# Performance work log

Hardware: AMD Instinct MI355X
Metric: run time of the kernel (lower is better)

The kernel has to match this reference:

```python
import jax, jax.numpy as jnp
import numpy as np

B, T, C, H, HS = 2, 2048, 1024, 16, 64
W_SIZE = 128
BLK = 64
NB = T // BLK            # 32 blocks
NSEL = 8                 # selected blocks per (b, h)
EPS = 1e-8


def setup_inputs() -> dict:
    key = jax.random.key(0)
    ks = jax.random.split(key, 12)
    s = 0.02
    return {
        "hidden_states": jax.random.normal(ks[0], (B, T, C), dtype=jnp.float32),
        "Wq": jax.random.normal(ks[1], (C, C), dtype=jnp.float32) * s,
        "bq": jnp.zeros((C,), jnp.float32),
        "Wk": jax.random.normal(ks[2], (C, C), dtype=jnp.float32) * s,
        "bk": jnp.zeros((C,), jnp.float32),
        "Wv": jax.random.normal(ks[3], (C, C), dtype=jnp.float32) * s,
        "bv": jnp.zeros((C,), jnp.float32),
        "Wo": jax.random.normal(ks[4], (C, C), dtype=jnp.float32) * s,
        "bo": jnp.zeros((C,), jnp.float32),
        "Wg": jax.random.normal(ks[5], (C, 3), dtype=jnp.float32) * s,
        "bg": jnp.zeros((3,), jnp.float32),
    }


def _sdpa(q, k, v, mask):
    # q: [B,H,Tq,HS], k/v: [B,H,S,HS], mask: [Tq,S] bool (True = attend)
    scale = 1.0 / jnp.sqrt(jnp.asarray(HS, q.dtype))
    scores = jnp.einsum('bhqd,bhkd->bhqk', q, k) * scale
    scores = jnp.where(mask, scores, jnp.asarray(-jnp.inf, scores.dtype))
    return jnp.einsum('bhqk,bhkd->bhqd', jax.nn.softmax(scores, axis=-1), v)


def _forward(x, Wq, bq, Wk, bk, Wv, bv, Wo, bo, Wg, bg):
    q = (x @ Wq + bq).reshape(B, T, H, HS).transpose(0, 2, 1, 3)
    k = (x @ Wk + bk).reshape(B, T, H, HS).transpose(0, 2, 1, 3)
    v = (x @ Wv + bv).reshape(B, T, H, HS).transpose(0, 2, 1, 3)

    gates = jax.nn.softmax(x @ Wg + bg, axis=-1)  # [B,T,3]
    g_sl, g_sel, g_cmp = gates[..., 0:1], gates[..., 1:2], gates[..., 2:3]

    i = jnp.arange(T)[:, None]

    # --- sliding-window branch (causal AND within window band) ---
    j = jnp.arange(T)[None, :]
    slide_mask = (j <= i) & (i - j <= W_SIZE)
    out_sl = _sdpa(q, k, v, slide_mask)

    # --- block representatives (mean-pooled K/V blocks) ---
    kb = k.reshape(B, H, NB, BLK, HS)
    vb = v.reshape(B, H, NB, BLK, HS)
    k_rep = kb.mean(axis=3)  # [B,H,NB,HS]

    # cosine similarity of each query vs each block rep, averaged over T
    qn = q / jnp.maximum(jnp.linalg.norm(q, axis=-1, keepdims=True), EPS)
    kn = k_rep / jnp.maximum(jnp.linalg.norm(k_rep, axis=-1, keepdims=True), EPS)
    global_scores = jnp.einsum('bhtd,bhnd->bhtn', qn, kn).mean(axis=2)  # [B,H,NB]
    _, top_idx = jax.lax.top_k(global_scores, NSEL)  # [B,H,NSEL]

    # gather selected K/V blocks
    sel_k = jnp.take_along_axis(kb, top_idx[..., None, None], axis=2).reshape(B, H, NSEL * BLK, HS)
    sel_v = jnp.take_along_axis(vb, top_idx[..., None, None], axis=2).reshape(B, H, NSEL * BLK, HS)

    # torch is_causal with Tq != S is top-left aligned: allow j <= i
    js = jnp.arange(NSEL * BLK)[None, :]
    out_sel = _sdpa(q, sel_k, sel_v, js <= i)

    # --- compressed branch over block reps ---
    v_cmp = vb.mean(axis=3)  # [B,H,NB,HS]
    jc = jnp.arange(NB)[None, :]
    out_cmp = _sdpa(q, k_rep, v_cmp, jc <= i)

    def merge(o):
        return o.transpose(0, 2, 1, 3).reshape(B, T, C)

    out = g_sl * merge(out_sl) + g_sel * merge(out_sel) + g_cmp * merge(out_cmp)
    return out @ Wo + bo


def reference(hidden_states, Wq, bq, Wk, bk, Wv, bv, Wo, bo, Wg, bg):
    return _forward(hidden_states, Wq, bq, Wk, bk, Wv, bv, Wo, bo, Wg, bg)
```

## Files before the change

kernel.cpp:

```cpp
#include <hip/hip_runtime.h>
#include <hip/hip_bf16.h>
#include <math.h>

#define Bc   2
#define Tc   2048
#define Cc   1024
#define Hc   16
#define HSc  64
#define WSZ  128
#define BLKc 64
#define NBc  32
#define NSELc 8
#define Mrows (Bc*Tc)
#define QCH  32
#define LST  88
#define LSTP 68
#define MAXT 12
#define SOFT_C 4.0f

typedef __attribute__((ext_vector_type(8))) _Float16 half8;
typedef __attribute__((ext_vector_type(4))) float f32x4v;
typedef __attribute__((ext_vector_type(8))) unsigned short ushort8v;

__device__ __forceinline__ float wave_sum(float v) {
    #pragma unroll
    for (int o = 32; o; o >>= 1) v += __shfl_xor(v, o);
    return v;
}

__device__ __forceinline__ unsigned short f2h(float f) {
    _Float16 h = (_Float16)f;
    unsigned short u;
    __builtin_memcpy(&u, &h, 2);
    return u;
}
__device__ __forceinline__ float h2f(unsigned short u) {
    _Float16 h;
    __builtin_memcpy(&h, &u, 2);
    return (float)h;
}

__device__ __forceinline__ void gload16(const void* g, void* l) {
    __builtin_amdgcn_global_load_lds(
        (const __attribute__((address_space(1))) void*)g,
        (__attribute__((address_space(3))) void*)l, 16, 0, 0);
}

__global__ __launch_bounds__(256)
void cvt_gates_kernel(const float* __restrict__ x, unsigned short* __restrict__ xb,
                      const float* __restrict__ Wg, const float* __restrict__ bg,
                      float* __restrict__ gates)
{
    if (blockIdx.x < 4096) {
        int i = (blockIdx.x * 256 + threadIdx.x) * 4;
        float4 v = *(const float4*)&x[i];
        ushort4 o;
        o.x = f2h(v.x); o.y = f2h(v.y); o.z = f2h(v.z); o.w = f2h(v.w);
        *(ushort4*)&xb[i] = o;
        return;
    }
    const int row  = (blockIdx.x - 4096) * 4 + (threadIdx.x >> 6);
    const int lane = threadIdx.x & 63;
    const float* xr = x + (size_t)row * Cc;
    float p0 = 0, p1 = 0, p2 = 0;
    #pragma unroll
    for (int it = 0; it < 4; ++it) {
        int k4 = lane * 4 + it * 256;
        float4 xv = *(const float4*)&xr[k4];
        float4 w0 = *(const float4*)&Wg[k4 * 3];
        float4 w1 = *(const float4*)&Wg[k4 * 3 + 4];
        float4 w2 = *(const float4*)&Wg[k4 * 3 + 8];
        p0 += xv.x * w0.x + xv.y * w0.w + xv.z * w1.z + xv.w * w2.y;
        p1 += xv.x * w0.y + xv.y * w1.x + xv.z * w1.w + xv.w * w2.z;
        p2 += xv.x * w0.z + xv.y * w1.y + xv.z * w2.x + xv.w * w2.w;
    }
    p0 = wave_sum(p0); p1 = wave_sum(p1); p2 = wave_sum(p2);
    if (lane == 0) {
        p0 += bg[0]; p1 += bg[1]; p2 += bg[2];
        float m = fmaxf(p0, fmaxf(p1, p2));
        float e0 = expf(p0 - m), e1 = expf(p1 - m), e2 = expf(p2 - m);
        float s = e0 + e1 + e2;
        gates[row * 3 + 0] = e0 / s;
        gates[row * 3 + 1] = e1 / s;
        gates[row * 3 + 2] = e2 / s;
    }
}

__global__ __launch_bounds__(256)
void cvt_wT4_kernel(const float* __restrict__ W0, const float* __restrict__ W1,
                    const float* __restrict__ W2, const float* __restrict__ W3,
                    unsigned short* __restrict__ D012, unsigned short* __restrict__ D3)
{
    __shared__ float tile[64][65];
    const int z = blockIdx.z;
    const float* W = (z == 0) ? W0 : (z == 1) ? W1 : (z == 2) ? W2 : W3;
    unsigned short* WT = (z < 3) ? (D012 + (size_t)z * 1024 * 1024) : D3;
    const int n0 = blockIdx.x * 64, k0 = blockIdx.y * 64;
    const int tid = threadIdx.x;
    #pragma unroll
    for (int it = 0; it < 16; ++it) {
        int lin = tid + it * 256;
        int r = lin >> 6, c = lin & 63;
        tile[r][c] = W[(size_t)(k0 + r) * 1024 + n0 + c];
    }
    __syncthreads();
    #pragma unroll
    for (int it = 0; it < 16; ++it) {
        int lin = tid + it * 256;
        int n = lin >> 6, k = lin & 63;
        WT[(size_t)(n0 + n) * 1024 + k0 + k] = f2h(tile[k][n]);
    }
}


#define FENCE asm volatile("" ::: "memory")
#define BAR() do { FENCE; __builtin_amdgcn_s_barrier(); FENCE; } while(0)
#define WAIT_LGKM0() do { asm volatile("s_waitcnt lgkmcnt(0)" ::: "memory"); \
                          __builtin_amdgcn_sched_barrier(0); } while(0)
#define WAIT_VM(N) do { asm volatile("s_waitcnt vmcnt(" #N ")" ::: "memory"); } while(0)

#define LDA(BUF, MH) do { \
    const unsigned short* _p = &lds[BUF][0][(wmo + (MH)*64 + r16) * 64]; \
    a0[0] = *(const half8*)(_p +        cc0); a1[0] = *(const half8*)(_p +        cc1); \
    a0[1] = *(const half8*)(_p + 1024 + cc0); a1[1] = *(const half8*)(_p + 1024 + cc1); \
    a0[2] = *(const half8*)(_p + 2048 + cc0); a1[2] = *(const half8*)(_p + 2048 + cc1); \
    a0[3] = *(const half8*)(_p + 3072 + cc0); a1[3] = *(const half8*)(_p + 3072 + cc1); \
} while(0)

#define LDB(BUF, NH) do { \
    const unsigned short* _p = &lds[BUF][1][(wno + (NH)*32 + r16) * 64]; \
    b0[0] = *(const half8*)(_p +        cc0); b1[0] = *(const half8*)(_p +        cc1); \
    b0[1] = *(const half8*)(_p + 1024 + cc0); b1[1] = *(const half8*)(_p + 1024 + cc1); \
} while(0)

#define CLP(I, J, MH, NH) \
    acc[(MH)*4+(I)][(NH)*2+(J)] = __builtin_amdgcn_mfma_f32_16x16x32_f16(a0[I], b0[J], acc[(MH)*4+(I)][(NH)*2+(J)], 0, 0, 0); \
    acc[(MH)*4+(I)][(NH)*2+(J)] = __builtin_amdgcn_mfma_f32_16x16x32_f16(a1[I], b1[J], acc[(MH)*4+(I)][(NH)*2+(J)], 0, 0, 0);
#define CL(MH, NH) do { \
    __builtin_amdgcn_s_setprio(1); \
    CLP(0,0,MH,NH) CLP(0,1,MH,NH) CLP(1,0,MH,NH) CLP(1,1,MH,NH) \
    CLP(2,0,MH,NH) CLP(2,1,MH,NH) CLP(3,0,MH,NH) CLP(3,1,MH,NH) \
    __builtin_amdgcn_s_setprio(0); \
} while(0)

#define STAGEA(BUF, G, TILE) do { \
    size_t _co = (size_t)(TILE) * 64 + scol_x; \
    gload16(Ag + (size_t)(m0 +       (G)*64 + wid*8 + l8) * 1024 + _co, \
            &lds[BUF][0][((G)*64 + wid*8) * 64]); \
    gload16(Ag + (size_t)(m0 + 128 + (G)*64 + wid*8 + l8) * 1024 + _co, \
            &lds[BUF][0][(128 + (G)*64 + wid*8) * 64]); \
} while(0)

#define STAGEB(BUF, G, TILE) do { \
    size_t _co = (size_t)(TILE) * 64 + scol_x; \
    int _r0 = (wid >> 2) * 64 + (G)*32 + (wid & 3) * 8; \
    gload16(BTg + (size_t)(n0 +       _r0 + l8) * 1024 + _co, \
            &lds[BUF][1][_r0 * 64]); \
    gload16(BTg + (size_t)(n0 + 128 + _r0 + l8) * 1024 + _co, \
            &lds[BUF][1][(128 + _r0) * 64]); \
} while(0)

__global__ __launch_bounds__(512, 2)
void mfma_gemm_qkv8(const unsigned short* __restrict__ Ag,
                    const unsigned short* __restrict__ BTg,
                    const float* __restrict__ bq, const float* __restrict__ bk,
                    const float* __restrict__ bv,
                    unsigned short* __restrict__ Qh, unsigned short* __restrict__ Kf,
                    unsigned short* __restrict__ Vf)
{
    __shared__ unsigned short lds[2][2][256 * 64];
    const int tid  = threadIdx.x;
    const int lane = tid & 63, wid = tid >> 6;
    const int quad = lane >> 4, r16 = lane & 15;
    const int m0 = blockIdx.y * 256, n0 = blockIdx.x * 256;
    const int wmo = (wid >> 2) * 128;
    const int wno = (wid & 3) * 64;
    const int l8 = lane >> 3;
    const int scol_x = ((lane & 7) ^ l8) * 8;
    const int xsw = (r16 & 7) * 8;
    const int cc0 = (quad * 8) ^ xsw;
    const int cc1 = (32 + quad * 8) ^ xsw;

    f32x4v acc[8][4];
    #pragma unroll
    for (int i = 0; i < 8; ++i)
        #pragma unroll
        for (int j = 0; j < 4; ++j)
            acc[i][j] = (f32x4v){0.f, 0.f, 0.f, 0.f};

    half8 a0[4], a1[4], b0[2], b1[2];

    STAGEA(0, 0, 0); STAGEB(0, 1, 0); STAGEA(0, 1, 0); STAGEB(0, 0, 0);
    STAGEA(1, 0, 1); STAGEB(1, 1, 1);
    WAIT_VM(4);
    BAR();

    for (int it = 0; it < 8; ++it) {
        const int t1 = 2 * it + 1, t2v = 2 * it + 2, t3v = 2 * it + 3;
        const bool s2 = (t2v < 16), s3 = (t3v < 16);
        LDA(0, 0); LDB(0, 0);
        STAGEA(1, 1, t1);
        BAR(); WAIT_LGKM0();
        CL(0, 0);
        BAR();
        LDB(0, 1);
        STAGEB(1, 0, t1);
        BAR(); WAIT_LGKM0();
        CL(0, 1);
        BAR();
        LDA(0, 1);
        if (s2) STAGEA(0, 0, t2v);
        BAR(); WAIT_LGKM0();
        CL(1, 1);
        BAR();
        LDB(0, 0);
        if (s2) STAGEB(0, 1, t2v);
        BAR(); WAIT_LGKM0();
        CL(1, 0);
        if (it == 7) { WAIT_VM(0); } else { WAIT_VM(4); }
        BAR();
        LDA(1, 0); LDB(1, 0);
        if (s2) STAGEA(0, 1, t2v);
        BAR(); WAIT_LGKM0();
        CL(0, 0);
        BAR();
        LDB(1, 1);
        if (s2) STAGEB(0, 0, t2v);
        BAR(); WAIT_LGKM0();
        CL(0, 1);
        BAR();
        LDA(1, 1);
        if (s3) STAGEA(1, 0, t3v);
        BAR(); WAIT_LGKM0();
        CL(1, 1);
        BAR();
        LDB(1, 0);
        if (s3) STAGEB(1, 1, t3v);
        BAR(); WAIT_LGKM0();
        CL(1, 0);
        if (it < 7) WAIT_VM(4);
        BAR();
    }

    const int which = n0 >> 10;
    const float* bias = (which == 0) ? bq : ((which == 1) ? bk : bv);
    unsigned short* dst = (which == 0) ? Qh : ((which == 1) ? Kf : Vf);
    const float sc = (which == 0) ? 0.125f : 1.0f;
    #pragma unroll
    for (int i = 0; i < 8; ++i) {
        int mbase = m0 + wmo + i * 16 + quad * 4;
        #pragma unroll
        for (int j = 0; j < 4; ++j) {
            int n = n0 + wno + j * 16 + r16;
            int nn = n & 1023;
            float bvv = bias[nn];
            int h = nn >> 6, d = nn & 63;
            #pragma unroll
            for (int r = 0; r < 4; ++r) {
                int m = mbase + r;
                int b = m >> 11, t = m & 2047;
                float v = (acc[i][j][r] + bvv) * sc;
                dst[(((size_t)(b * Hc + h) * Tc) + t) * HSc + d] = f2h(v);
            }
        }
    }
}

__global__ __launch_bounds__(256)
void mfma_gemm_kernel(const unsigned short* __restrict__ A,
                      const unsigned short* __restrict__ BT,
                      const float* __restrict__ bias,
                      float* __restrict__ Y)
{
    constexpr int K = 1024;
    __shared__ unsigned short As[4 * 64 * 8];
    __shared__ unsigned short Bs[4 * 128 * 8];
    const int tid  = threadIdx.x;
    const int lane = tid & 63;
    const int wid  = tid >> 6;
    const int m0 = blockIdx.y * 64, n0 = blockIdx.x * 128;
    const int wm = (wid >> 1) * 32, wn = (wid & 1) * 64;

    f32x4v acc[2][4];
    #pragma unroll
    for (int i = 0; i < 2; ++i)
        #pragma unroll
        for (int j = 0; j < 4; ++j)
            acc[i][j] = (f32x4v){0.f, 0.f, 0.f, 0.f};

    const int kq_r = lane >> 4;
    const int r16  = lane & 15;

    for (int k0 = 0; k0 < K; k0 += 32) {
        __syncthreads();
        gload16(A + (size_t)(m0 + lane) * K + k0 + wid * 8,
                As + (size_t)(wid * 64) * 8);
        #pragma unroll
        for (int it = 0; it < 2; ++it) {
            int cell = wid * 64 + it * 256 + lane;
            int kq = cell >> 7, row = cell & 127;
            gload16(BT + (size_t)(n0 + row) * K + k0 + kq * 8,
                    Bs + (size_t)(wid * 64 + it * 256) * 8);
        }
        __syncthreads();

        half8 af[2], bf[4];
        #pragma unroll
        for (int i = 0; i < 2; ++i)
            af[i] = *(const half8*)&As[(size_t)(kq_r * 64 + wm + i * 16 + r16) * 8];
        #pragma unroll
        for (int j = 0; j < 4; ++j)
            bf[j] = *(const half8*)&Bs[(size_t)(kq_r * 128 + wn + j * 16 + r16) * 8];
        #pragma unroll
        for (int i = 0; i < 2; ++i)
            #pragma unroll
            for (int j = 0; j < 4; ++j)
                acc[i][j] = __builtin_amdgcn_mfma_f32_16x16x32_f16(af[i], bf[j], acc[i][j], 0, 0, 0);
    }

    #pragma unroll
    for (int i = 0; i < 2; ++i) {
        int mbase = m0 + wm + i * 16 + (lane >> 4) * 4;
        #pragma unroll
        for (int j = 0; j < 4; ++j) {
            int n = n0 + wn + j * 16 + (lane & 15);
            float bv = bias[n];
            #pragma unroll
            for (int r = 0; r < 4; ++r)
                Y[(size_t)(mbase + r) * 1024 + n] = acc[i][j][r] + bv;
        }
    }
}

__global__ __launch_bounds__(256)
void vtrans_stats_kernel(const unsigned short* __restrict__ Kf,
                         const unsigned short* __restrict__ Vf,
                         unsigned short* __restrict__ Vt,
                         float* __restrict__ krep,
                         unsigned short* __restrict__ krep16,
                         unsigned short* __restrict__ vcmpT16)
{
    __shared__ unsigned short vtile[64][65];
    __shared__ unsigned short ktile[64][65];
    const int nb = blockIdx.x, bh = blockIdx.y;
    const int t0 = nb * BLKc;
    const int tid = threadIdx.x;
    const int c4 = (tid & 15) * 4, r = tid >> 4;
    const unsigned short* vsrc = Vf + ((size_t)bh * Tc + t0) * HSc;
    const unsigned short* ksrc = Kf + ((size_t)bh * Tc + t0) * HSc;
    #pragma unroll
    for (int it = 0; it < 4; ++it) {
        int tt = r + it * 16;
        *(ushort4*)&vtile[tt][c4] = *(const ushort4*)&vsrc[(size_t)tt * HSc + c4];
        *(ushort4*)&ktile[tt][c4] = *(const ushort4*)&ksrc[(size_t)tt * HSc + c4];
    }
    __syncthreads();
    unsigned short* dst = Vt + (size_t)bh * HSc * Tc + t0;
    #pragma unroll
    for (int it = 0; it < 4; ++it) {
        int d = r + it * 16;
        ushort4 o;
        o.x = vtile[c4 + 0][d]; o.y = vtile[c4 + 1][d];
        o.z = vtile[c4 + 2][d]; o.w = vtile[c4 + 3][d];
        *(ushort4*)&dst[(size_t)d * Tc + c4] = o;
    }
    if (tid < 64) {
        const int d = tid;
        float sk = 0.f, sv = 0.f;
        #pragma unroll 8
        for (int t = 0; t < BLKc; ++t) {
            sk += h2f(ktile[t][d]);
            sv += h2f(vtile[t][d]);
        }
        float km = sk * (1.0f / BLKc), vm = sv * (1.0f / BLKc);
        krep[((size_t)bh * NBc + nb) * HSc + d] = km;
        krep16[(size_t)bh * 4096 + nb * 64 + d] = f2h(km);
        krep16[(size_t)bh * 4096 + (nb + 32) * 64 + d] = 0;
        vcmpT16[(size_t)bh * 4096 + d * 64 + nb] = f2h(vm);
        vcmpT16[(size_t)bh * 4096 + d * 64 + nb + 32] = 0;
    }
}

__global__ __launch_bounds__(64)
void qbar_part_kernel(const unsigned short* __restrict__ Qh, float* __restrict__ qpart)
{
    __shared__ float rinv[64];
    const int ch = blockIdx.x, bh = blockIdx.y, lane = threadIdx.x;
    const int t0 = ch * (Tc / QCH);
    const unsigned short* qbase = Qh + ((size_t)bh * Tc + t0) * HSc;

    {
        const unsigned short* qr = qbase + (size_t)lane * HSc;
        float ss = 0.f;
        #pragma unroll
        for (int d8 = 0; d8 < 8; ++d8) {
            ushort8v v8 = *(const ushort8v*)&qr[d8 * 8];
            #pragma unroll
            for (int j = 0; j < 8; ++j) { float f = h2f(v8[j]); ss += f * f; }
        }
        rinv[lane] = 1.0f / fmaxf(sqrtf(ss), 1e-8f);
    }
    __syncthreads();

    float acc = 0.f;
    #pragma unroll 8
    for (int t = 0; t < 64; ++t)
        acc += h2f(qbase[(size_t)t * HSc + lane]) * rinv[t];
    qpart[((size_t)bh * QCH + ch) * HSc + lane] = acc;
}

__global__ __launch_bounds__(64)
void topk_kernel(const float* __restrict__ qpart, const float* __restrict__ krep,
                 int* __restrict__ topidx)
{
    int bh = blockIdx.x, lane = threadIdx.x;
    __shared__ float sc[NBc];
    __shared__ float qbs[HSc];
    float qa = 0.0f;
    #pragma unroll
    for (int c = 0; c < QCH; c++)
        qa += qpart[((size_t)bh * QCH + c) * HSc + lane];
    qbs[lane] = qa * (1.0f / Tc);
    __syncthreads();
    if (lane < NBc) {
        float dot = 0, nk = 0;
        for (int d = 0; d < HSc; d++) {
            float kv = krep[((size_t)bh * NBc + lane) * HSc + d];
            nk += kv * kv;
            dot += qbs[d] * kv;
        }
        sc[lane] = dot / fmaxf(sqrtf(nk), 1e-8f);
    }
    __syncthreads();
    if (lane == 0) {
        for (int s = 0; s < NSELc; s++) {
            int best = 0; float bv = sc[0];
            for (int n = 1; n < NBc; n++)
                if (sc[n] > bv) { bv = sc[n]; best = n; }
            topidx[bh * NSELc + s] = best;
            sc[best] = -INFINITY;
        }
    }
}

__device__ __forceinline__ void attn_tile3(
    int p0, int wlim, int klim, int qg0,
    const unsigned short* __restrict__ Kh, const unsigned short* __restrict__ Vt,
    unsigned short* __restrict__ Ph,
    half8 aq0, half8 aq1, half8 ones, int wq, int l16, int quad,
    f32x4v o[4], f32x4v& o5)
{
    f32x4v s[4];
    #pragma unroll
    for (int t = 0; t < 4; ++t) {
        f32x4v sa = (f32x4v){0.f, 0.f, 0.f, 0.f};
        half8 b0 = *(const half8*)&Kh[(t * 16 + l16) * LST + quad * 8];
        half8 b1 = *(const half8*)&Kh[(t * 16 + l16) * LST + 32 + quad * 8];
        sa = __builtin_amdgcn_mfma_f32_16x16x32_f16(aq0, b0, sa, 0, 0, 0);
        sa = __builtin_amdgcn_mfma_f32_16x16x32_f16(aq1, b1, sa, 0, 0, 0);
        s[t] = sa;
    }

    #pragma unroll
    for (int t = 0; t < 4; ++t) {
        int kk = t * 16 + l16;
        bool kok = kk < klim;
        int jt = p0 + kk;
        #pragma unroll
        for (int r = 0; r < 4; ++r) {
            int q = qg0 + r;
            bool valid = kok && (jt <= q) && (q - jt <= wlim);
            float p = valid ? __expf(s[t][r] - SOFT_C) : 0.0f;
            Ph[(wq + quad * 4 + r) * LSTP + t * 16 + l16] = f2h(p);
        }
    }


    half8 ap0 = *(const half8*)&Ph[(wq + l16) * LSTP + quad * 8];
    half8 ap1 = *(const half8*)&Ph[(wq + l16) * LSTP + 32 + quad * 8];
    o5 = __builtin_amdgcn_mfma_f32_16x16x32_f16(ap0, ones, o5, 0, 0, 0);
    o5 = __builtin_amdgcn_mfma_f32_16x16x32_f16(ap1, ones, o5, 0, 0, 0);
    #pragma unroll
    for (int dt = 0; dt < 4; ++dt) {
        half8 v0 = *(const half8*)&Vt[(dt * 16 + l16) * LST + quad * 8];
        half8 v1 = *(const half8*)&Vt[(dt * 16 + l16) * LST + 32 + quad * 8];
        o[dt] = __builtin_amdgcn_mfma_f32_16x16x32_f16(ap0, v0, o[dt], 0, 0, 0);
        o[dt] = __builtin_amdgcn_mfma_f32_16x16x32_f16(ap1, v1, o[dt], 0, 0, 0);
    }
}

__global__ __launch_bounds__(256)
void fattn_kernel(const unsigned short* __restrict__ Qh16,
                  const unsigned short* __restrict__ Kf,
                  const unsigned short* __restrict__ Vtg,
                  const unsigned short* __restrict__ krep16,
                  const unsigned short* __restrict__ vcmpT16,
                  const int* __restrict__ topidx,
                  const float* __restrict__ gates, unsigned short* __restrict__ merged)
{
    __shared__ unsigned short KH[2][64 * LST];
    __shared__ unsigned short VT[2][64 * LST];
    __shared__ unsigned short Ph[64 * LSTP];
    __shared__ float gsl[3 * 64];
    __shared__ int tKb[MAXT], tP0[MAXT], tWl[MAXT], tKl[MAXT], tBid[MAXT];

    const int qt = blockIdx.x;
    const int bh = blockIdx.y;
    const int b  = bh >> 4, h = bh & 15;
    const int tid  = threadIdx.x;
    const int wid  = tid >> 6, lane = tid & 63;
    const int l16  = lane & 15, quad = lane >> 4;
    const int q0 = qt * 64;
    const int wq = wid * 16;
    const int qg0 = q0 + wq + quad * 4;

    const int nslide = (qt < 2 ? qt : 2) + 1;
    const int nsel   = (qt + 1 < NSELc) ? (qt + 1) : NSELc;
    const int nt     = nslide + nsel + 1;

    half8 aq0, aq1, ones;
    {
        const unsigned short* qrow = Qh16 + ((size_t)bh * Tc + q0 + wq + l16) * HSc;
        aq0 = *(const half8*)(qrow + quad * 8);
        aq1 = *(const half8*)(qrow + 32 + quad * 8);
        #pragma unroll
        for (int j = 0; j < 8; ++j) ones[j] = (_Float16)1.0f;
    }

    if (tid < 64) {
        size_t gb = ((size_t)b * Tc + q0 + tid) * 3;
        gsl[0 * 64 + tid] = gates[gb + 0];
        gsl[1 * 64 + tid] = gates[gb + 1];
        gsl[2 * 64 + tid] = gates[gb + 2];
    }
    if (tid < nt) {
        int i = tid, kb, p0, wl, kl, bid;
        if (i < nslide)            { int tb = q0 - (nslide - 1 - i) * 64;
                                     kb = tb; p0 = tb; wl = WSZ; kl = 64; bid = 0; }
        else if (i < nslide + nsel){ int s = i - nslide;
                                     kb = topidx[bh * NSELc + s] * BLKc;
                                     p0 = s * BLKc; wl = 1 << 30; kl = 64; bid = 1; }
        else                       { kb = 0; p0 = 0; wl = 1 << 30; kl = NBc; bid = 2; }
        tKb[i] = kb; tP0[i] = p0; tWl[i] = wl; tKl[i] = kl; tBid[i] = bid;
    }

    f32x4v o[4], macc[4];
    f32x4v o5 = (f32x4v){0.f, 0.f, 0.f, 0.f};
    #pragma unroll
    for (int dt = 0; dt < 4; ++dt) {
        o[dt]    = (f32x4v){0.f, 0.f, 0.f, 0.f};
        macc[dt] = (f32x4v){0.f, 0.f, 0.f, 0.f};
    }

    const int seg = tid & 7, r0 = tid >> 3;
    const unsigned short* kbh = Kf  + (size_t)bh * Tc * HSc;
    const unsigned short* vbh = Vtg + (size_t)bh * HSc * Tc;

    {
        int tb0 = q0 - (nslide - 1) * 64;
        const unsigned short* kp = kbh + (size_t)tb0 * HSc;
        const unsigned short* vp = vbh + tb0;
        ushort8v k0 = *(const ushort8v*)(kp + (size_t)r0 * HSc + seg * 8);
        ushort8v k1 = *(const ushort8v*)(kp + (size_t)(r0 + 32) * HSc + seg * 8);
        ushort8v v0 = *(const ushort8v*)(vp + (size_t)r0 * Tc + seg * 8);
        ushort8v v1 = *(const ushort8v*)(vp + (size_t)(r0 + 32) * Tc + seg * 8);
        *(ushort8v*)&KH[0][r0 * LST + seg * 8] = k0;
        *(ushort8v*)&KH[0][(r0 + 32) * LST + seg * 8] = k1;
        *(ushort8v*)&VT[0][r0 * LST + seg * 8] = v0;
        *(ushort8v*)&VT[0][(r0 + 32) * LST + seg * 8] = v1;
    }
    __syncthreads();

    int pb = 0;
    for (int i = 0; i < nt; ++i) {
        const int cb = i & 1;
        const bool pf = (i + 1 < nt);
        ushort8v k0, k1, v0, v1;
        if (pf) {
            int bid2 = tBid[i + 1], kb2 = tKb[i + 1];
            const unsigned short *kp, *vp;
            int vs;
            if (bid2 < 2) { kp = kbh + (size_t)kb2 * HSc; vp = vbh + kb2; vs = Tc; }
            else          { kp = krep16 + (size_t)bh * 4096;
                            vp = vcmpT16 + (size_t)bh * 4096; vs = 64; }
            k0 = *(const ushort8v*)(kp + (size_t)r0 * HSc + seg * 8);
            k1 = *(const ushort8v*)(kp + (size_t)(r0 + 32) * HSc + seg * 8);
            v0 = *(const ushort8v*)(vp + (size_t)r0 * vs + seg * 8);
            v1 = *(const ushort8v*)(vp + (size_t)(r0 + 32) * vs + seg * 8);
        }
        int bid = tBid[i];
        if (bid != pb) {
            #pragma unroll
            for (int r = 0; r < 4; ++r) {
                float inv = gsl[pb * 64 + wq + quad * 4 + r] / o5[r];
                #pragma unroll
                for (int dt = 0; dt < 4; ++dt) { macc[dt][r] += inv * o[dt][r]; o[dt][r] = 0.f; }
                o5[r] = 0.f;
            }
            pb = bid;
        }
        attn_tile3(tP0[i], tWl[i], tKl[i], qg0, KH[cb], VT[cb], Ph,
                   aq0, aq1, ones, wq, l16, quad, o, o5);
        if (pf) {
            *(ushort8v*)&KH[cb ^ 1][r0 * LST + seg * 8] = k0;
            *(ushort8v*)&KH[cb ^ 1][(r0 + 32) * LST + seg * 8] = k1;
            *(ushort8v*)&VT[cb ^ 1][r0 * LST + seg * 8] = v0;
            *(ushort8v*)&VT[cb ^ 1][(r0 + 32) * LST + seg * 8] = v1;
        }
        __syncthreads();
    }
    #pragma unroll
    for (int r = 0; r < 4; ++r) {
        float inv = gsl[pb * 64 + wq + quad * 4 + r] / o5[r];
        #pragma unroll
        for (int dt = 0; dt < 4; ++dt) macc[dt][r] += inv * o[dt][r];
    }

    #pragma unroll
    for (int r = 0; r < 4; ++r) {
        size_t mrow = (size_t)b * Tc + qg0 + r;
        #pragma unroll
        for (int dt = 0; dt < 4; ++dt)
            merged[mrow * Cc + h * HSc + dt * 16 + l16] = f2h(macc[dt][r]);
    }
}

extern "C" void kernel_launch(void* const* d_in, const int* in_sizes, int n_in,
                              void* d_out, int out_size, void* d_ws, size_t ws_size,
                              hipStream_t stream)
{
    const float* x  = (const float*)d_in[0];
    const float* Wq = (const float*)d_in[1];
    const float* bq = (const float*)d_in[2];
    const float* Wk = (const float*)d_in[3];
    const float* bk = (const float*)d_in[4];
    const float* Wv = (const float*)d_in[5];
    const float* bv = (const float*)d_in[6];
    const float* Wo = (const float*)d_in[7];
    const float* bo = (const float*)d_in[8];
    const float* Wg = (const float*)d_in[9];
    const float* bg = (const float*)d_in[10];
    float* out = (float*)d_out;
    float* ws  = (float*)d_ws;

    unsigned short* Qh16 = (unsigned short*)(ws + 0);
    unsigned short* Kf16 = (unsigned short*)(ws + 2097152);
    unsigned short* Vf16 = (unsigned short*)(ws + 4194304);
    unsigned short* Vt16 = (unsigned short*)(ws + 6291456);
    unsigned short* Mgb  = (unsigned short*)(ws + 8388608);
    unsigned short* xb   = (unsigned short*)(ws + 10485760);
    unsigned short* WqkvT = (unsigned short*)(ws + 12582912);
    unsigned short* WoT   = (unsigned short*)(ws + 14155776);
    float* gates = ws + 14680064;
    float* krep  = ws + 14692352;
    unsigned short* krep16  = (unsigned short*)(ws + 14757888);
    unsigned short* vcmpT16 = (unsigned short*)(ws + 14823424);
    float* qpart = ws + 14888960;
    int*   topidx = (int*)(ws + 14954496);

    cvt_gates_kernel<<<4096 + Mrows / 4, 256, 0, stream>>>(x, xb, Wg, bg, gates);
    cvt_wT4_kernel<<<dim3(16, 16, 4), 256, 0, stream>>>(Wq, Wk, Wv, Wo, WqkvT, WoT);

    mfma_gemm_qkv8<<<dim3(12, 16), 512, 0, stream>>>(xb, WqkvT, bq, bk, bv,
                                                     Qh16, Kf16, Vf16);
    vtrans_stats_kernel<<<dim3(NBc, Bc * Hc), 256, 0, stream>>>(Kf16, Vf16, Vt16,
                                                                krep, krep16, vcmpT16);
    qbar_part_kernel<<<dim3(QCH, Bc * Hc), 64, 0, stream>>>(Qh16, qpart);
    topk_kernel<<<Bc * Hc, 64, 0, stream>>>(qpart, krep, topidx);
    fattn_kernel<<<dim3(Tc / 64, Bc * Hc), 256, 0, stream>>>(Qh16, Kf16, Vt16,
                                                             krep16, vcmpT16,
                                                             topidx, gates, Mgb);
    mfma_gemm_kernel<<<dim3(8, 64), 256, 0, stream>>>(Mgb, WoT, bo, out);
}
```

Measured before the change: 233.9 us.

## Load attention K/V fragments directly from global memory into registers

Removes the shared-memory double-buffered K/V staging and the per-tile block-wide barriers from the fused attention kernel. Each wave now loads its MFMA operand fragments for K and V straight from global memory (relying on L1/L2 for reuse across the four waves), computes the tile descriptors inline, and reads gates directly. Occupancy is raised via launch bounds and smaller LDS. The trade is redundant global loads per wave and no explicit prefetch overlap, with load latency exposed before each tile's MFMAs.

```diff
diff --git a/kernel.cpp b/kernel.cpp
--- a/kernel.cpp
+++ b/kernel.cpp
@@ -13,9 +13,7 @@
 #define NSELc 8
 #define Mrows (Bc*Tc)
 #define QCH  32
-#define LST  88
 #define LSTP 68
-#define MAXT 12
 #define SOFT_C 4.0f
 
 typedef __attribute__((ext_vector_type(8))) _Float16 half8;
@@ -443,53 +441,7 @@
     }
 }
 
-__device__ __forceinline__ void attn_tile3(
-    int p0, int wlim, int klim, int qg0,
-    const unsigned short* __restrict__ Kh, const unsigned short* __restrict__ Vt,
-    unsigned short* __restrict__ Ph,
-    half8 aq0, half8 aq1, half8 ones, int wq, int l16, int quad,
-    f32x4v o[4], f32x4v& o5)
-{
-    f32x4v s[4];
-    #pragma unroll
-    for (int t = 0; t < 4; ++t) {
-        f32x4v sa = (f32x4v){0.f, 0.f, 0.f, 0.f};
-        half8 b0 = *(const half8*)&Kh[(t * 16 + l16) * LST + quad * 8];
-        half8 b1 = *(const half8*)&Kh[(t * 16 + l16) * LST + 32 + quad * 8];
-        sa = __builtin_amdgcn_mfma_f32_16x16x32_f16(aq0, b0, sa, 0, 0, 0);
-        sa = __builtin_amdgcn_mfma_f32_16x16x32_f16(aq1, b1, sa, 0, 0, 0);
-        s[t] = sa;
-    }
-
-    #pragma unroll
-    for (int t = 0; t < 4; ++t) {
-        int kk = t * 16 + l16;
-        bool kok = kk < klim;
-        int jt = p0 + kk;
-        #pragma unroll
-        for (int r = 0; r < 4; ++r) {
-            int q = qg0 + r;
-            bool valid = kok && (jt <= q) && (q - jt <= wlim);
-            float p = valid ? __expf(s[t][r] - SOFT_C) : 0.0f;
-            Ph[(wq + quad * 4 + r) * LSTP + t * 16 + l16] = f2h(p);
-        }
-    }
-
-
-    half8 ap0 = *(const half8*)&Ph[(wq + l16) * LSTP + quad * 8];
-    half8 ap1 = *(const half8*)&Ph[(wq + l16) * LSTP + 32 + quad * 8];
-    o5 = __builtin_amdgcn_mfma_f32_16x16x32_f16(ap0, ones, o5, 0, 0, 0);
-    o5 = __builtin_amdgcn_mfma_f32_16x16x32_f16(ap1, ones, o5, 0, 0, 0);
-    #pragma unroll
-    for (int dt = 0; dt < 4; ++dt) {
-        half8 v0 = *(const half8*)&Vt[(dt * 16 + l16) * LST + quad * 8];
-        half8 v1 = *(const half8*)&Vt[(dt * 16 + l16) * LST + 32 + quad * 8];
-        o[dt] = __builtin_amdgcn_mfma_f32_16x16x32_f16(ap0, v0, o[dt], 0, 0, 0);
-        o[dt] = __builtin_amdgcn_mfma_f32_16x16x32_f16(ap1, v1, o[dt], 0, 0, 0);
-    }
-}
-
-__global__ __launch_bounds__(256)
+__global__ __launch_bounds__(256, 3)
 void fattn_kernel(const unsigned short* __restrict__ Qh16,
                   const unsigned short* __restrict__ Kf,
                   const unsigned short* __restrict__ Vtg,
@@ -498,11 +450,7 @@
                   const int* __restrict__ topidx,
                   const float* __restrict__ gates, unsigned short* __restrict__ merged)
 {
-    __shared__ unsigned short KH[2][64 * LST];
-    __shared__ unsigned short VT[2][64 * LST];
     __shared__ unsigned short Ph[64 * LSTP];
-    __shared__ float gsl[3 * 64];
-    __shared__ int tKb[MAXT], tP0[MAXT], tWl[MAXT], tKl[MAXT], tBid[MAXT];
 
     const int qt = blockIdx.x;
     const int bh = blockIdx.y;
@@ -527,23 +475,6 @@
         for (int j = 0; j < 8; ++j) ones[j] = (_Float16)1.0f;
     }
 
-    if (tid < 64) {
-        size_t gb = ((size_t)b * Tc + q0 + tid) * 3;
-        gsl[0 * 64 + tid] = gates[gb + 0];
-        gsl[1 * 64 + tid] = gates[gb + 1];
-        gsl[2 * 64 + tid] = gates[gb + 2];
-    }
-    if (tid < nt) {
-        int i = tid, kb, p0, wl, kl, bid;
-        if (i < nslide)            { int tb = q0 - (nslide - 1 - i) * 64;
-                                     kb = tb; p0 = tb; wl = WSZ; kl = 64; bid = 0; }
-        else if (i < nslide + nsel){ int s = i - nslide;
-                                     kb = topidx[bh * NSELc + s] * BLKc;
-                                     p0 = s * BLKc; wl = 1 << 30; kl = 64; bid = 1; }
-        else                       { kb = 0; p0 = 0; wl = 1 << 30; kl = NBc; bid = 2; }
-        tKb[i] = kb; tP0[i] = p0; tWl[i] = wl; tKl[i] = kl; tBid[i] = bid;
-    }
-
     f32x4v o[4], macc[4];
     f32x4v o5 = (f32x4v){0.f, 0.f, 0.f, 0.f};
     #pragma unroll
@@ -552,66 +483,89 @@
         macc[dt] = (f32x4v){0.f, 0.f, 0.f, 0.f};
     }
 
-    const int seg = tid & 7, r0 = tid >> 3;
     const unsigned short* kbh = Kf  + (size_t)bh * Tc * HSc;
     const unsigned short* vbh = Vtg + (size_t)bh * HSc * Tc;
-
-    {
-        int tb0 = q0 - (nslide - 1) * 64;
-        const unsigned short* kp = kbh + (size_t)tb0 * HSc;
-        const unsigned short* vp = vbh + tb0;
-        ushort8v k0 = *(const ushort8v*)(kp + (size_t)r0 * HSc + seg * 8);
-        ushort8v k1 = *(const ushort8v*)(kp + (size_t)(r0 + 32) * HSc + seg * 8);
-        ushort8v v0 = *(const ushort8v*)(vp + (size_t)r0 * Tc + seg * 8);
-        ushort8v v1 = *(const ushort8v*)(vp + (size_t)(r0 + 32) * Tc + seg * 8);
-        *(ushort8v*)&KH[0][r0 * LST + seg * 8] = k0;
-        *(ushort8v*)&KH[0][(r0 + 32) * LST + seg * 8] = k1;
-        *(ushort8v*)&VT[0][r0 * LST + seg * 8] = v0;
-        *(ushort8v*)&VT[0][(r0 + 32) * LST + seg * 8] = v1;
-    }
-    __syncthreads();
+    const int lofs = l16 * 64 + quad * 8;
 
     int pb = 0;
     for (int i = 0; i < nt; ++i) {
-        const int cb = i & 1;
-        const bool pf = (i + 1 < nt);
-        ushort8v k0, k1, v0, v1;
-        if (pf) {
-            int bid2 = tBid[i + 1], kb2 = tKb[i + 1];
-            const unsigned short *kp, *vp;
-            int vs;
-            if (bid2 < 2) { kp = kbh + (size_t)kb2 * HSc; vp = vbh + kb2; vs = Tc; }
-            else          { kp = krep16 + (size_t)bh * 4096;
-                            vp = vcmpT16 + (size_t)bh * 4096; vs = 64; }
-            k0 = *(const ushort8v*)(kp + (size_t)r0 * HSc + seg * 8);
-            k1 = *(const ushort8v*)(kp + (size_t)(r0 + 32) * HSc + seg * 8);
-            v0 = *(const ushort8v*)(vp + (size_t)r0 * vs + seg * 8);
-            v1 = *(const ushort8v*)(vp + (size_t)(r0 + 32) * vs + seg * 8);
-        }
-        int bid = tBid[i];
+        const bool iscmp = (i == nt - 1);
+        int kb, p0, wl, kl, bid;
+        if (i < nslide)       { int tb = q0 - (nslide - 1 - i) * 64;
+                                kb = tb; p0 = tb; wl = WSZ; kl = 64; bid = 0; }
+        else if (!iscmp)      { int s = i - nslide;
+                                kb = topidx[bh * NSELc + s] * BLKc;
+                                p0 = s * BLKc; wl = 1 << 30; kl = 64; bid = 1; }
+        else                  { kb = 0; p0 = 0; wl = 1 << 30; kl = NBc; bid = 2; }
+
+        const unsigned short* kpl = (iscmp ? krep16 + (size_t)bh * 4096
+                                           : kbh + (size_t)kb * HSc) + lofs;
+        half8 bk0[4], bk1[4], bv0[4], bv1[4];
+        #pragma unroll
+        for (int t = 0; t < 4; ++t) {
+            bk0[t] = *(const half8*)(kpl + t * 1024);
+            bk1[t] = *(const half8*)(kpl + t * 1024 + 32);
+        }
+        const unsigned short* vpl;
+        size_t vr16;
+        if (iscmp) { vpl = vcmpT16 + (size_t)bh * 4096 + lofs;            vr16 = 1024; }
+        else       { vpl = vbh + kb + (size_t)l16 * Tc + quad * 8;        vr16 = (size_t)16 * Tc; }
+        #pragma unroll
+        for (int dt = 0; dt < 4; ++dt) {
+            bv0[dt] = *(const half8*)(vpl + dt * vr16);
+            bv1[dt] = *(const half8*)(vpl + dt * vr16 + 32);
+        }
+
         if (bid != pb) {
             #pragma unroll
             for (int r = 0; r < 4; ++r) {
-                float inv = gsl[pb * 64 + wq + quad * 4 + r] / o5[r];
+                float g = gates[((size_t)b * Tc + qg0 + r) * 3 + pb];
+                float inv = g / o5[r];
                 #pragma unroll
                 for (int dt = 0; dt < 4; ++dt) { macc[dt][r] += inv * o[dt][r]; o[dt][r] = 0.f; }
                 o5[r] = 0.f;
             }
             pb = bid;
         }
-        attn_tile3(tP0[i], tWl[i], tKl[i], qg0, KH[cb], VT[cb], Ph,
-                   aq0, aq1, ones, wq, l16, quad, o, o5);
-        if (pf) {
-            *(ushort8v*)&KH[cb ^ 1][r0 * LST + seg * 8] = k0;
-            *(ushort8v*)&KH[cb ^ 1][(r0 + 32) * LST + seg * 8] = k1;
-            *(ushort8v*)&VT[cb ^ 1][r0 * LST + seg * 8] = v0;
-            *(ushort8v*)&VT[cb ^ 1][(r0 + 32) * LST + seg * 8] = v1;
-        }
-        __syncthreads();
-    }
+
+        f32x4v s[4];
+        #pragma unroll
+        for (int t = 0; t < 4; ++t) {
+            f32x4v sa = (f32x4v){0.f, 0.f, 0.f, 0.f};
+            sa = __builtin_amdgcn_mfma_f32_16x16x32_f16(aq0, bk0[t], sa, 0, 0, 0);
+            sa = __builtin_amdgcn_mfma_f32_16x16x32_f16(aq1, bk1[t], sa, 0, 0, 0);
+            s[t] = sa;
+        }
+
+        #pragma unroll
+        for (int t = 0; t < 4; ++t) {
+            int kk = t * 16 + l16;
+            bool kok = kk < kl;
+            int jt = p0 + kk;
+            #pragma unroll
+            for (int r = 0; r < 4; ++r) {
+                int q = qg0 + r;
+                bool valid = kok && (jt <= q) && (q - jt <= wl);
+                float p = valid ? __expf(s[t][r] - SOFT_C) : 0.0f;
+                Ph[(wq + quad * 4 + r) * LSTP + t * 16 + l16] = f2h(p);
+            }
+        }
+
+        half8 ap0 = *(const half8*)&Ph[(wq + l16) * LSTP + quad * 8];
+        half8 ap1 = *(const half8*)&Ph[(wq + l16) * LSTP + 32 + quad * 8];
+        o5 = __builtin_amdgcn_mfma_f32_16x16x32_f16(ap0, ones, o5, 0, 0, 0);
+        o5 = __builtin_amdgcn_mfma_f32_16x16x32_f16(ap1, ones, o5, 0, 0, 0);
+        #pragma unroll
+        for (int dt = 0; dt < 4; ++dt) {
+            o[dt] = __builtin_amdgcn_mfma_f32_16x16x32_f16(ap0, bv0[dt], o[dt], 0, 0, 0);
+            o[dt] = __builtin_amdgcn_mfma_f32_16x16x32_f16(ap1, bv1[dt], o[dt], 0, 0, 0);
+        }
+    }
+
     #pragma unroll
     for (int r = 0; r < 4; ++r) {
-        float inv = gsl[pb * 64 + wq + quad * 4 + r] / o5[r];
+        float g = gates[((size_t)b * Tc + qg0 + r) * 3 + 2];
+        float inv = g / o5[r];
         #pragma unroll
         for (int dt = 0; dt < 4; ++dt) macc[dt][r] += inv * o[dt][r];
     }
```

New measurement: 271.5 us. 16.1% more time.

## Swizzle LDS tiles, skip masking on full tiles, drop shared metadata tables

Applied to the files above, without the earlier changes.

Replaces the padded LDS strides for the K, V and P tiles with unpadded 64-wide rows and an XOR swizzle, aiming to avoid bank conflicts while using less LDS. Adds a no-mask fast path for tiles that are fully visible. Computes tile metadata inline instead of staging it in shared tables, reads gates straight from global memory, and sets launch bounds to request 4 blocks per SM. The smaller LDS footprint may raise occupancy, at the cost of more index arithmetic and scattered global gate loads.

```diff
diff --git a/kernel.cpp b/kernel.cpp
--- a/kernel.cpp
+++ b/kernel.cpp
@@ -13,9 +13,6 @@
 #define NSELc 8
 #define Mrows (Bc*Tc)
 #define QCH  32
-#define LST  88
-#define LSTP 68
-#define MAXT 12
 #define SOFT_C 4.0f
 
 typedef __attribute__((ext_vector_type(8))) _Float16 half8;
@@ -443,53 +440,68 @@
     }
 }
 
-__device__ __forceinline__ void attn_tile3(
-    int p0, int wlim, int klim, int qg0,
+__device__ __forceinline__ void attn_tile4(
+    int p0, int wlim, int klim, int qg0, bool nomask,
     const unsigned short* __restrict__ Kh, const unsigned short* __restrict__ Vt,
     unsigned short* __restrict__ Ph,
     half8 aq0, half8 aq1, half8 ones, int wq, int l16, int quad,
+    int kc0, int kc1,
     f32x4v o[4], f32x4v& o5)
 {
     f32x4v s[4];
     #pragma unroll
     for (int t = 0; t < 4; ++t) {
         f32x4v sa = (f32x4v){0.f, 0.f, 0.f, 0.f};
-        half8 b0 = *(const half8*)&Kh[(t * 16 + l16) * LST + quad * 8];
-        half8 b1 = *(const half8*)&Kh[(t * 16 + l16) * LST + 32 + quad * 8];
+        half8 b0 = *(const half8*)&Kh[(t * 16 + l16) * 64 + kc0];
+        half8 b1 = *(const half8*)&Kh[(t * 16 + l16) * 64 + kc1];
         sa = __builtin_amdgcn_mfma_f32_16x16x32_f16(aq0, b0, sa, 0, 0, 0);
         sa = __builtin_amdgcn_mfma_f32_16x16x32_f16(aq1, b1, sa, 0, 0, 0);
         s[t] = sa;
     }
 
-    #pragma unroll
-    for (int t = 0; t < 4; ++t) {
-        int kk = t * 16 + l16;
-        bool kok = kk < klim;
-        int jt = p0 + kk;
-        #pragma unroll
-        for (int r = 0; r < 4; ++r) {
-            int q = qg0 + r;
-            bool valid = kok && (jt <= q) && (q - jt <= wlim);
-            float p = valid ? __expf(s[t][r] - SOFT_C) : 0.0f;
-            Ph[(wq + quad * 4 + r) * LSTP + t * 16 + l16] = f2h(p);
-        }
-    }
-
-
-    half8 ap0 = *(const half8*)&Ph[(wq + l16) * LSTP + quad * 8];
-    half8 ap1 = *(const half8*)&Ph[(wq + l16) * LSTP + 32 + quad * 8];
+    const int prow = wq + quad * 4;
+    if (nomask) {
+        #pragma unroll
+        for (int t = 0; t < 4; ++t) {
+            int c = t * 16 + l16;
+            #pragma unroll
+            for (int r = 0; r < 4; ++r) {
+                float p = __expf(s[t][r] - SOFT_C);
+                Ph[(prow + r) * 64 + (c ^ (((prow + r) & 7) * 8))] = f2h(p);
+            }
+        }
+    } else {
+        #pragma unroll
+        for (int t = 0; t < 4; ++t) {
+            int kk = t * 16 + l16;
+            bool kok = kk < klim;
+            int jt = p0 + kk;
+            #pragma unroll
+            for (int r = 0; r < 4; ++r) {
+                int q = qg0 + r;
+                bool valid = kok && (jt <= q) && (q - jt <= wlim);
+                float p = valid ? __expf(s[t][r] - SOFT_C) : 0.0f;
+                Ph[(prow + r) * 64 + (kk ^ (((prow + r) & 7) * 8))] = f2h(p);
+            }
+        }
+    }
+
+
+    const int prd = (wq + l16) * 64;
+    half8 ap0 = *(const half8*)&Ph[prd + kc0];
+    half8 ap1 = *(const half8*)&Ph[prd + kc1];
     o5 = __builtin_amdgcn_mfma_f32_16x16x32_f16(ap0, ones, o5, 0, 0, 0);
     o5 = __builtin_amdgcn_mfma_f32_16x16x32_f16(ap1, ones, o5, 0, 0, 0);
     #pragma unroll
     for (int dt = 0; dt < 4; ++dt) {
-        half8 v0 = *(const half8*)&Vt[(dt * 16 + l16) * LST + quad * 8];
-        half8 v1 = *(const half8*)&Vt[(dt * 16 + l16) * LST + 32 + quad * 8];
+        half8 v0 = *(const half8*)&Vt[(dt * 16 + l16) * 64 + kc0];
+        half8 v1 = *(const half8*)&Vt[(dt * 16 + l16) * 64 + kc1];
         o[dt] = __builtin_amdgcn_mfma_f32_16x16x32_f16(ap0, v0, o[dt], 0, 0, 0);
         o[dt] = __builtin_amdgcn_mfma_f32_16x16x32_f16(ap1, v1, o[dt], 0, 0, 0);
     }
 }
 
-__global__ __launch_bounds__(256)
+__global__ __launch_bounds__(256, 4)
 void fattn_kernel(const unsigned short* __restrict__ Qh16,
                   const unsigned short* __restrict__ Kf,
                   const unsigned short* __restrict__ Vtg,
@@ -498,11 +510,9 @@
                   const int* __restrict__ topidx,
                   const float* __restrict__ gates, unsigned short* __restrict__ merged)
 {
-    __shared__ unsigned short KH[2][64 * LST];
-    __shared__ unsigned short VT[2][64 * LST];
-    __shared__ unsigned short Ph[64 * LSTP];
-    __shared__ float gsl[3 * 64];
-    __shared__ int tKb[MAXT], tP0[MAXT], tWl[MAXT], tKl[MAXT], tBid[MAXT];
+    __shared__ unsigned short KH[2][64 * 64];
+    __shared__ unsigned short VT[2][64 * 64];
+    __shared__ unsigned short Ph[64 * 64];
 
     const int qt = blockIdx.x;
     const int bh = blockIdx.y;
@@ -527,23 +537,6 @@
         for (int j = 0; j < 8; ++j) ones[j] = (_Float16)1.0f;
     }
 
-    if (tid < 64) {
-        size_t gb = ((size_t)b * Tc + q0 + tid) * 3;
-        gsl[0 * 64 + tid] = gates[gb + 0];
-        gsl[1 * 64 + tid] = gates[gb + 1];
-        gsl[2 * 64 + tid] = gates[gb + 2];
-    }
-    if (tid < nt) {
-        int i = tid, kb, p0, wl, kl, bid;
-        if (i < nslide)            { int tb = q0 - (nslide - 1 - i) * 64;
-                                     kb = tb; p0 = tb; wl = WSZ; kl = 64; bid = 0; }
-        else if (i < nslide + nsel){ int s = i - nslide;
-                                     kb = topidx[bh * NSELc + s] * BLKc;
-                                     p0 = s * BLKc; wl = 1 << 30; kl = 64; bid = 1; }
-        else                       { kb = 0; p0 = 0; wl = 1 << 30; kl = NBc; bid = 2; }
-        tKb[i] = kb; tP0[i] = p0; tWl[i] = wl; tKl[i] = kl; tBid[i] = bid;
-    }
-
     f32x4v o[4], macc[4];
     f32x4v o5 = (f32x4v){0.f, 0.f, 0.f, 0.f};
     #pragma unroll
@@ -553,6 +546,13 @@
     }
 
     const int seg = tid & 7, r0 = tid >> 3;
+    const int stc = (seg ^ (r0 & 7)) * 8;
+    const int st0 = r0 * 64 + stc;
+    const int st1 = (r0 + 32) * 64 + stc;
+    const int psw = (l16 & 7) * 8;
+    const int kc0 = (quad * 8) ^ psw;
+    const int kc1 = (32 + quad * 8) ^ psw;
+
     const unsigned short* kbh = Kf  + (size_t)bh * Tc * HSc;
     const unsigned short* vbh = Vtg + (size_t)bh * HSc * Tc;
 
@@ -560,14 +560,10 @@
         int tb0 = q0 - (nslide - 1) * 64;
         const unsigned short* kp = kbh + (size_t)tb0 * HSc;
         const unsigned short* vp = vbh + tb0;
-        ushort8v k0 = *(const ushort8v*)(kp + (size_t)r0 * HSc + seg * 8);
-        ushort8v k1 = *(const ushort8v*)(kp + (size_t)(r0 + 32) * HSc + seg * 8);
-        ushort8v v0 = *(const ushort8v*)(vp + (size_t)r0 * Tc + seg * 8);
-        ushort8v v1 = *(const ushort8v*)(vp + (size_t)(r0 + 32) * Tc + seg * 8);
-        *(ushort8v*)&KH[0][r0 * LST + seg * 8] = k0;
-        *(ushort8v*)&KH[0][(r0 + 32) * LST + seg * 8] = k1;
-        *(ushort8v*)&VT[0][r0 * LST + seg * 8] = v0;
-        *(ushort8v*)&VT[0][(r0 + 32) * LST + seg * 8] = v1;
+        *(ushort8v*)&KH[0][st0] = *(const ushort8v*)(kp + (size_t)r0 * HSc + seg * 8);
+        *(ushort8v*)&KH[0][st1] = *(const ushort8v*)(kp + (size_t)(r0 + 32) * HSc + seg * 8);
+        *(ushort8v*)&VT[0][st0] = *(const ushort8v*)(vp + (size_t)r0 * Tc + seg * 8);
+        *(ushort8v*)&VT[0][st1] = *(const ushort8v*)(vp + (size_t)(r0 + 32) * Tc + seg * 8);
     }
     __syncthreads();
 
@@ -577,7 +573,11 @@
         const bool pf = (i + 1 < nt);
         ushort8v k0, k1, v0, v1;
         if (pf) {
-            int bid2 = tBid[i + 1], kb2 = tKb[i + 1];
+            const int i2 = i + 1;
+            int kb2, bid2;
+            if (i2 < nslide)            { kb2 = q0 - (nslide - 1 - i2) * 64; bid2 = 0; }
+            else if (i2 < nslide + nsel){ kb2 = topidx[bh * NSELc + (i2 - nslide)] * BLKc; bid2 = 1; }
+            else                        { kb2 = 0; bid2 = 2; }
             const unsigned short *kp, *vp;
             int vs;
             if (bid2 < 2) { kp = kbh + (size_t)kb2 * HSc; vp = vbh + kb2; vs = Tc; }
@@ -588,30 +588,44 @@
             v0 = *(const ushort8v*)(vp + (size_t)r0 * vs + seg * 8);
             v1 = *(const ushort8v*)(vp + (size_t)(r0 + 32) * vs + seg * 8);
         }
-        int bid = tBid[i];
+
+        int p0v, wl, kl, bid; bool nomask;
+        if (i < nslide)            { int tb = q0 - (nslide - 1 - i) * 64;
+                                     p0v = tb; wl = WSZ; kl = 64; bid = 0;
+                                     nomask = (tb == q0 - 64); }
+        else if (i < nslide + nsel){ int s = i - nslide;
+                                     p0v = s * BLKc; wl = 1 << 30; kl = 64; bid = 1;
+                                     nomask = (p0v + 63 < q0); }
+        else                       { p0v = 0; wl = 1 << 30; kl = NBc; bid = 2;
+                                     nomask = false; }
+
         if (bid != pb) {
             #pragma unroll
             for (int r = 0; r < 4; ++r) {
-                float inv = gsl[pb * 64 + wq + quad * 4 + r] / o5[r];
+                float g = gates[((size_t)b * Tc + qg0 + r) * 3 + pb];
+                float inv = g / o5[r];
                 #pragma unroll
                 for (int dt = 0; dt < 4; ++dt) { macc[dt][r] += inv * o[dt][r]; o[dt][r] = 0.f; }
                 o5[r] = 0.f;
             }
             pb = bid;
         }
-        attn_tile3(tP0[i], tWl[i], tKl[i], qg0, KH[cb], VT[cb], Ph,
-                   aq0, aq1, ones, wq, l16, quad, o, o5);
+
+        attn_tile4(p0v, wl, kl, qg0, nomask, KH[cb], VT[cb], Ph,
+                   aq0, aq1, ones, wq, l16, quad, kc0, kc1, o, o5);
+
         if (pf) {
-            *(ushort8v*)&KH[cb ^ 1][r0 * LST + seg * 8] = k0;
-            *(ushort8v*)&KH[cb ^ 1][(r0 + 32) * LST + seg * 8] = k1;
-            *(ushort8v*)&VT[cb ^ 1][r0 * LST + seg * 8] = v0;
-            *(ushort8v*)&VT[cb ^ 1][(r0 + 32) * LST + seg * 8] = v1;
+            *(ushort8v*)&KH[cb ^ 1][st0] = k0;
+            *(ushort8v*)&KH[cb ^ 1][st1] = k1;
+            *(ushort8v*)&VT[cb ^ 1][st0] = v0;
+            *(ushort8v*)&VT[cb ^ 1][st1] = v1;
         }
         __syncthreads();
     }
     #pragma unroll
     for (int r = 0; r < 4; ++r) {
-        float inv = gsl[pb * 64 + wq + quad * 4 + r] / o5[r];
+        float g = gates[((size_t)b * Tc + qg0 + r) * 3 + 2];
+        float inv = g / o5[r];
         #pragma unroll
         for (int dt = 0; dt < 4; ++dt) macc[dt][r] += inv * o[dt][r];
     }
```

Result: faster. 214.5 us (-8.3%).
